# Optimization experiments

Hardware: AMD Instinct MI355X
Metric: run time of the kernel (lower is better)

The kernel has to match this reference:

```python
import jax, jax.numpy as jnp
import numpy as np

NUM_USERS = 100000
NUM_ITEMS = 150000
NUM_BRANDS = 5000
NUM_NODES = NUM_USERS + NUM_ITEMS + NUM_BRANDS
EMBED_DIM = 64
N_LAYERS = 3
NUM_EDGES = 2000000


def setup_inputs() -> dict:
    key = jax.random.key(0)
    k1, k2, k3, k4, k5, k6 = jax.random.split(key, 6)
    # xavier_uniform bound for Embedding weight [n, d]
    def xavier(k, n, d):
        bound = float(np.sqrt(6.0 / (n + d)))
        return jax.random.uniform(k, (n, d), dtype=jnp.float32, minval=-bound, maxval=bound)
    user_emb = xavier(k1, NUM_USERS, EMBED_DIM)
    item_emb = xavier(k2, NUM_ITEMS, EMBED_DIM)
    brand_emb = xavier(k3, NUM_BRANDS, EMBED_DIM)
    adj_rows = jax.random.randint(k4, (NUM_EDGES,), 0, NUM_NODES, dtype=jnp.int32)
    adj_cols = jax.random.randint(k5, (NUM_EDGES,), 0, NUM_NODES, dtype=jnp.int32)
    # normalized adjacency values (positive, small), as in sym-normalized LightGCN adj
    adj_vals = jax.random.uniform(k6, (NUM_EDGES,), dtype=jnp.float32) * 0.1
    return {
        "user_emb": user_emb,
        "item_emb": item_emb,
        "brand_emb": brand_emb,
        "adj_rows": adj_rows,
        "adj_cols": adj_cols,
        "adj_vals": adj_vals,
    }


def _spmm(rows, cols, vals, x):
    # y[r] = sum_{e: rows[e]==r} vals[e] * x[cols[e]]
    msgs = vals[:, None] * x[cols]  # [E, D]
    return jax.ops.segment_sum(msgs, rows, num_segments=NUM_NODES)


def reference(user_emb, item_emb, brand_emb, adj_rows, adj_cols, adj_vals):
    ego = jnp.concatenate([user_emb, item_emb, brand_emb], axis=0)  # [N, D]
    acc = ego  # running sum instead of stack+mean
    for _ in range(N_LAYERS):
        ego = _spmm(adj_rows, adj_cols, adj_vals, ego)
        acc = acc + ego
    final = acc / jnp.float32(N_LAYERS + 1)
    final_user = final[:NUM_USERS]
    final_item = final[NUM_USERS:NUM_USERS + NUM_ITEMS]
    return (final_user, final_item)
```

## Files before the change

kernel.cpp:

```cpp
#include <hip/hip_runtime.h>

#define NUSER 100000
#define NITEM 150000
#define NBRAND 5000
#define NNODES (NUSER + NITEM + NBRAND)
#define DIM 64
#define NOUTROWS (NUSER + NITEM)

#define BINSHIFT 10
#define NBINS ((NNODES + (1 << BINSHIFT) - 1) >> BINSHIFT)
#define EPB 8192
#define CAP 12288

__device__ __forceinline__ float bf2f(unsigned short u) {
    union { unsigned int i; float f; } c;
    c.i = ((unsigned int)u) << 16;
    return c.f;
}
__device__ __forceinline__ unsigned short f2bf(float f) {
    union { float f; unsigned int i; } c;
    c.f = f;
    unsigned int r = c.i + 0x7FFFu + ((c.i >> 16) & 1u);
    return (unsigned short)(r >> 16);
}

__global__ __launch_bounds__(256) void lgcn_binA_init(const int* __restrict__ rows,
                                                      const int* __restrict__ cols,
                                                      const float* __restrict__ vals,
                                                      int* __restrict__ binCnt,
                                                      int2* __restrict__ binned,
                                                      int nedges, int nBinABlocks,
                                                      const float4* __restrict__ u,
                                                      const float4* __restrict__ it,
                                                      const float4* __restrict__ br,
                                                      ushort4* __restrict__ x0b) {
    __shared__ int hist[NBINS];
    __shared__ int base[NBINS];
    if (blockIdx.x >= nBinABlocks) {
        int i = (blockIdx.x - nBinABlocks) * 256 + threadIdx.x;
        const int total = NNODES * (DIM / 4);
        if (i >= total) return;
        float4 v;
        if (i < NUSER * (DIM / 4)) {
            v = u[i];
        } else if (i < (NUSER + NITEM) * (DIM / 4)) {
            v = it[i - NUSER * (DIM / 4)];
        } else {
            v = br[i - (NUSER + NITEM) * (DIM / 4)];
        }
        ushort4 o;
        o.x = f2bf(v.x); o.y = f2bf(v.y); o.z = f2bf(v.z); o.w = f2bf(v.w);
        x0b[i] = o;
        return;
    }
    for (int i = threadIdx.x; i < NBINS; i += 256) hist[i] = 0;
    __syncthreads();
    int beg = blockIdx.x * EPB;
    int end = beg + EPB;
    if (end > nedges) end = nedges;
    for (int e = beg + threadIdx.x; e < end; e += 256) {
        atomicAdd(&hist[rows[e] >> BINSHIFT], 1);
    }
    __syncthreads();
    for (int i = threadIdx.x; i < NBINS; i += 256) {
        int h = hist[i];
        base[i] = h ? (i * CAP + atomicAdd(&binCnt[i], h)) : 0;
        hist[i] = 0;
    }
    __syncthreads();
    for (int e = beg + threadIdx.x; e < end; e += 256) {
        int r = rows[e];
        int b = r >> BINSHIFT;
        int pos = base[b] + atomicAdd(&hist[b], 1);
        int2 p;
        p.x = ((r & ((1 << BINSHIFT) - 1)) << 18) | cols[e];
        p.y = __float_as_int(vals[e]);
        binned[pos] = p;
    }
}

__global__ __launch_bounds__(256) void lgcn_binscan(const int* __restrict__ binCnt,
                                                    int* __restrict__ binScan,
                                                    int* __restrict__ rowptr, int nedges) {
    __shared__ int lds[256];
    int t = threadIdx.x;
    int v = (t < NBINS) ? binCnt[t] : 0;
    lds[t] = v;
    __syncthreads();
    for (int off = 1; off < 256; off <<= 1) {
        int s = (t >= off) ? lds[t - off] : 0;
        __syncthreads();
        lds[t] += s;
        __syncthreads();
    }
    if (t < NBINS) binScan[t] = lds[t] - v;
    if (t == 0) rowptr[NNODES] = nedges;
}

__global__ __launch_bounds__(256) void lgcn_binB(const int* __restrict__ binCnt,
                                                 const int* __restrict__ binScan,
                                                 const int2* __restrict__ binned,
                                                 int2* __restrict__ colval,
                                                 int* __restrict__ rowptr) {
    __shared__ int lhist[1024];
    __shared__ int lcur[1024];
    __shared__ int part[256];
    int b = blockIdx.x;
    int t = threadIdx.x;
    int cnt = binCnt[b];
    int gbase = binScan[b];
    int rbeg = b << BINSHIFT;
    int nrows = NNODES - rbeg;
    if (nrows > 1024) nrows = 1024;
    #pragma unroll
    for (int k = 0; k < 4; ++k) lhist[t + 256 * k] = 0;
    __syncthreads();
    const int2* bsrc = binned + (size_t)b * CAP;
    for (int e = t; e < cnt; e += 256) {
        atomicAdd(&lhist[bsrc[e].x >> 18], 1);
    }
    __syncthreads();
    int h0 = lhist[4 * t + 0];
    int h1 = lhist[4 * t + 1];
    int h2 = lhist[4 * t + 2];
    int h3 = lhist[4 * t + 3];
    int tot = h0 + h1 + h2 + h3;
    part[t] = tot;
    __syncthreads();
    for (int off = 1; off < 256; off <<= 1) {
        int v = (t >= off) ? part[t - off] : 0;
        __syncthreads();
        part[t] += v;
        __syncthreads();
    }
    int c0 = gbase + part[t] - tot;
    int c1 = c0 + h0;
    int c2 = c1 + h1;
    int c3 = c2 + h2;
    lcur[4 * t + 0] = c0;
    lcur[4 * t + 1] = c1;
    lcur[4 * t + 2] = c2;
    lcur[4 * t + 3] = c3;
    if (4 * t + 0 < nrows) rowptr[rbeg + 4 * t + 0] = c0;
    if (4 * t + 1 < nrows) rowptr[rbeg + 4 * t + 1] = c1;
    if (4 * t + 2 < nrows) rowptr[rbeg + 4 * t + 2] = c2;
    if (4 * t + 3 < nrows) rowptr[rbeg + 4 * t + 3] = c3;
    __syncthreads();
    for (int e = t; e < cnt; e += 256) {
        int2 p = bsrc[e];
        int lr = p.x >> 18;
        int pos = atomicAdd(&lcur[lr], 1);
        int2 cv;
        cv.x = p.x & 0x3FFFF;
        cv.y = p.y;
        colval[pos] = cv;
    }
}

template <bool FINAL>
__global__ __launch_bounds__(256) void lgcn_spmm_csr(const int* __restrict__ row_ptr,
                                                     const int2* __restrict__ colval,
                                                     const ushort4* __restrict__ xb,
                                                     ushort4* __restrict__ yb,
                                                     const ushort4* __restrict__ x0b,
                                                     const ushort4* __restrict__ y1b,
                                                     const ushort4* __restrict__ y2b,
                                                     float4* __restrict__ out) {
    int t = blockIdx.x * blockDim.x + threadIdx.x;
    int row = t >> 4;
    int l = t & 15;
    if (FINAL) { if (row >= NOUTROWS) return; }
    else       { if (row >= NNODES) return; }
    int beg = row_ptr[row];
    int end = row_ptr[row + 1];
    float4 s = make_float4(0.f, 0.f, 0.f, 0.f);
    int p = beg;
    while (p + 8 <= end) {
        int2 cv[8];
        ushort4 a[8];
        #pragma unroll
        for (int k = 0; k < 8; ++k) cv[k] = colval[p + k];
        #pragma unroll
        for (int k = 0; k < 8; ++k) a[k] = xb[(size_t)cv[k].x * (DIM / 4) + l];
        #pragma unroll
        for (int k = 0; k < 8; ++k) {
            float v = __int_as_float(cv[k].y);
            s.x += v * bf2f(a[k].x); s.y += v * bf2f(a[k].y);
            s.z += v * bf2f(a[k].z); s.w += v * bf2f(a[k].w);
        }
        p += 8;
    }
    if (p + 4 <= end) {
        int2 cv[4];
        ushort4 a[4];
        #pragma unroll
        for (int k = 0; k < 4; ++k) cv[k] = colval[p + k];
        #pragma unroll
        for (int k = 0; k < 4; ++k) a[k] = xb[(size_t)cv[k].x * (DIM / 4) + l];
        #pragma unroll
        for (int k = 0; k < 4; ++k) {
            float v = __int_as_float(cv[k].y);
            s.x += v * bf2f(a[k].x); s.y += v * bf2f(a[k].y);
            s.z += v * bf2f(a[k].z); s.w += v * bf2f(a[k].w);
        }
        p += 4;
    }
    if (p + 2 <= end) {
        int2 cv0 = colval[p];
        int2 cv1 = colval[p + 1];
        ushort4 a0 = xb[(size_t)cv0.x * (DIM / 4) + l];
        ushort4 a1 = xb[(size_t)cv1.x * (DIM / 4) + l];
        float v0 = __int_as_float(cv0.y);
        float v1 = __int_as_float(cv1.y);
        s.x += v0 * bf2f(a0.x); s.y += v0 * bf2f(a0.y);
        s.z += v0 * bf2f(a0.z); s.w += v0 * bf2f(a0.w);
        s.x += v1 * bf2f(a1.x); s.y += v1 * bf2f(a1.y);
        s.z += v1 * bf2f(a1.z); s.w += v1 * bf2f(a1.w);
        p += 2;
    }
    if (p < end) {
        int2 cv = colval[p];
        ushort4 a = xb[(size_t)cv.x * (DIM / 4) + l];
        float v = __int_as_float(cv.y);
        s.x += v * bf2f(a.x); s.y += v * bf2f(a.y);
        s.z += v * bf2f(a.z); s.w += v * bf2f(a.w);
    }
    size_t off = (size_t)row * (DIM / 4) + l;
    if (!FINAL) {
        ushort4 o;
        o.x = f2bf(s.x); o.y = f2bf(s.y); o.z = f2bf(s.z); o.w = f2bf(s.w);
        yb[off] = o;
    } else {
        ushort4 x0 = x0b[off];
        ushort4 a1 = y1b[off];
        ushort4 a2 = y2b[off];
        float4 r;
        r.x = (bf2f(x0.x) + bf2f(a1.x) + bf2f(a2.x) + s.x) * 0.25f;
        r.y = (bf2f(x0.y) + bf2f(a1.y) + bf2f(a2.y) + s.y) * 0.25f;
        r.z = (bf2f(x0.z) + bf2f(a1.z) + bf2f(a2.z) + s.z) * 0.25f;
        r.w = (bf2f(x0.w) + bf2f(a1.w) + bf2f(a2.w) + s.w) * 0.25f;
        out[off] = r;
    }
}


static inline size_t align256(size_t x) { return (x + 255) & ~(size_t)255; }

extern "C" void kernel_launch(void* const* d_in, const int* in_sizes, int n_in,
                              void* d_out, int out_size, void* d_ws, size_t ws_size,
                              hipStream_t stream) {
    const float4* u  = (const float4*)d_in[0];
    const float4* it = (const float4*)d_in[1];
    const float4* br = (const float4*)d_in[2];
    const int*   rows = (const int*)d_in[3];
    const int*   cols = (const int*)d_in[4];
    const float* vals = (const float*)d_in[5];
    const int nedges = in_sizes[3];
    float4* out = (float4*)d_out;

    char* ws = (char*)d_ws;
    size_t o = 0;
    ushort4* x0b   = (ushort4*)(ws + o); o = align256(o + (size_t)NNODES * DIM * 2);
    ushort4* y1b   = (ushort4*)(ws + o); o = align256(o + (size_t)NNODES * DIM * 2);
    ushort4* y2b   = (ushort4*)(ws + o); o = align256(o + (size_t)NNODES * DIM * 2);
    int*   rowptr  = (int*)(ws + o);     o = align256(o + (size_t)(NNODES + 1) * 4);
    int*   binCnt  = (int*)(ws + o);     o = align256(o + 256 * 4);
    int*   binScan = (int*)(ws + o);     o = align256(o + 256 * 4);
    int2*  colval  = (int2*)(ws + o);    o = align256(o + (size_t)nedges * 8);

    int2* binned = (int2*)y1b;

    const int THREADS = 256;
    const int vecTotal = NNODES * (DIM / 4);
    const int vecBlocks = (vecTotal + THREADS - 1) / THREADS;
    const int spmmBlocks = (NNODES * 16 + THREADS - 1) / THREADS;
    const int finalBlocks = (NOUTROWS * 16 + THREADS - 1) / THREADS;
    const int binABlocks = (nedges + EPB - 1) / EPB;

    hipMemsetAsync(binCnt, 0, 256 * 4, stream);
    lgcn_binA_init<<<binABlocks + vecBlocks, THREADS, 0, stream>>>(
        rows, cols, vals, binCnt, binned, nedges, binABlocks, u, it, br, x0b);
    lgcn_binscan<<<1, THREADS, 0, stream>>>(binCnt, binScan, rowptr, nedges);
    lgcn_binB<<<NBINS, THREADS, 0, stream>>>(binCnt, binScan, binned, colval, rowptr);

    lgcn_spmm_csr<false><<<spmmBlocks, THREADS, 0, stream>>>(rowptr, colval, x0b, y1b,
                                                             nullptr, nullptr, nullptr, nullptr);
    lgcn_spmm_csr<false><<<spmmBlocks, THREADS, 0, stream>>>(rowptr, colval, y1b, y2b,
                                                             nullptr, nullptr, nullptr, nullptr);
    lgcn_spmm_csr<true><<<finalBlocks, THREADS, 0, stream>>>(rowptr, colval, y2b, nullptr,
                                                             x0b, y1b, y2b, out);
}
```

Baseline: 238.6 us.

## Fold bin scan into binB, split init kernel, register-cache rows in binA

Removes the single-block bin-scan kernel; every binB block now does its own redundant 256-entry scan of the bin counts in shared memory. The fp32-to-bf16 conversion of the embeddings moves out of the binning kernel into its own launch after binB. binA now handles 4096 edges per block and keeps each thread's 16 row indices in registers, so rows are read from memory only once. This saves a launch and a global read pass, at the cost of an extra init launch, more binA blocks contending on the global bin counters, and repeated scan work in every binB block.

```diff
diff --git a/kernel.cpp b/kernel.cpp
--- a/kernel.cpp
+++ b/kernel.cpp
@@ -9,7 +9,7 @@
 
 #define BINSHIFT 10
 #define NBINS ((NNODES + (1 << BINSHIFT) - 1) >> BINSHIFT)
-#define EPB 8192
+#define EPB 4096
 #define CAP 12288
 
 __device__ __forceinline__ float bf2f(unsigned short u) {
@@ -24,42 +24,25 @@
     return (unsigned short)(r >> 16);
 }
 
-__global__ __launch_bounds__(256) void lgcn_binA_init(const int* __restrict__ rows,
-                                                      const int* __restrict__ cols,
-                                                      const float* __restrict__ vals,
-                                                      int* __restrict__ binCnt,
-                                                      int2* __restrict__ binned,
-                                                      int nedges, int nBinABlocks,
-                                                      const float4* __restrict__ u,
-                                                      const float4* __restrict__ it,
-                                                      const float4* __restrict__ br,
-                                                      ushort4* __restrict__ x0b) {
+__global__ __launch_bounds__(256) void lgcn_binA(const int* __restrict__ rows,
+                                                 const int* __restrict__ cols,
+                                                 const float* __restrict__ vals,
+                                                 int* __restrict__ binCnt,
+                                                 int2* __restrict__ binned,
+                                                 int nedges) {
     __shared__ int hist[NBINS];
     __shared__ int base[NBINS];
-    if (blockIdx.x >= nBinABlocks) {
-        int i = (blockIdx.x - nBinABlocks) * 256 + threadIdx.x;
-        const int total = NNODES * (DIM / 4);
-        if (i >= total) return;
-        float4 v;
-        if (i < NUSER * (DIM / 4)) {
-            v = u[i];
-        } else if (i < (NUSER + NITEM) * (DIM / 4)) {
-            v = it[i - NUSER * (DIM / 4)];
-        } else {
-            v = br[i - (NUSER + NITEM) * (DIM / 4)];
-        }
-        ushort4 o;
-        o.x = f2bf(v.x); o.y = f2bf(v.y); o.z = f2bf(v.z); o.w = f2bf(v.w);
-        x0b[i] = o;
-        return;
-    }
     for (int i = threadIdx.x; i < NBINS; i += 256) hist[i] = 0;
     __syncthreads();
     int beg = blockIdx.x * EPB;
     int end = beg + EPB;
     if (end > nedges) end = nedges;
-    for (int e = beg + threadIdx.x; e < end; e += 256) {
-        atomicAdd(&hist[rows[e] >> BINSHIFT], 1);
+    int r[16];
+    #pragma unroll
+    for (int k = 0; k < 16; ++k) {
+        int e = beg + threadIdx.x + k * 256;
+        r[k] = (e < end) ? rows[e] : -1;
+        if (r[k] >= 0) atomicAdd(&hist[r[k] >> BINSHIFT], 1);
     }
     __syncthreads();
     for (int i = threadIdx.x; i < NBINS; i += 256) {
@@ -68,53 +51,48 @@
         hist[i] = 0;
     }
     __syncthreads();
-    for (int e = beg + threadIdx.x; e < end; e += 256) {
-        int r = rows[e];
-        int b = r >> BINSHIFT;
-        int pos = base[b] + atomicAdd(&hist[b], 1);
-        int2 p;
-        p.x = ((r & ((1 << BINSHIFT) - 1)) << 18) | cols[e];
-        p.y = __float_as_int(vals[e]);
-        binned[pos] = p;
-    }
-}
-
-__global__ __launch_bounds__(256) void lgcn_binscan(const int* __restrict__ binCnt,
-                                                    int* __restrict__ binScan,
-                                                    int* __restrict__ rowptr, int nedges) {
-    __shared__ int lds[256];
-    int t = threadIdx.x;
-    int v = (t < NBINS) ? binCnt[t] : 0;
-    lds[t] = v;
-    __syncthreads();
-    for (int off = 1; off < 256; off <<= 1) {
-        int s = (t >= off) ? lds[t - off] : 0;
-        __syncthreads();
-        lds[t] += s;
-        __syncthreads();
-    }
-    if (t < NBINS) binScan[t] = lds[t] - v;
-    if (t == 0) rowptr[NNODES] = nedges;
+    #pragma unroll
+    for (int k = 0; k < 16; ++k) {
+        int e = beg + threadIdx.x + k * 256;
+        if (r[k] >= 0) {
+            int b = r[k] >> BINSHIFT;
+            int pos = base[b] + atomicAdd(&hist[b], 1);
+            int2 p;
+            p.x = ((r[k] & ((1 << BINSHIFT) - 1)) << 18) | cols[e];
+            p.y = __float_as_int(vals[e]);
+            binned[pos] = p;
+        }
+    }
 }
 
 __global__ __launch_bounds__(256) void lgcn_binB(const int* __restrict__ binCnt,
-                                                 const int* __restrict__ binScan,
                                                  const int2* __restrict__ binned,
                                                  int2* __restrict__ colval,
-                                                 int* __restrict__ rowptr) {
+                                                 int* __restrict__ rowptr,
+                                                 int nedges) {
     __shared__ int lhist[1024];
     __shared__ int lcur[1024];
     __shared__ int part[256];
+    __shared__ int sScan[256];
     int b = blockIdx.x;
     int t = threadIdx.x;
+    int v = (t < NBINS) ? binCnt[t] : 0;
+    sScan[t] = v;
+    #pragma unroll
+    for (int k = 0; k < 4; ++k) lhist[t + 256 * k] = 0;
+    __syncthreads();
+    for (int off = 1; off < 256; off <<= 1) {
+        int s2 = (t >= off) ? sScan[t - off] : 0;
+        __syncthreads();
+        sScan[t] += s2;
+        __syncthreads();
+    }
     int cnt = binCnt[b];
-    int gbase = binScan[b];
+    int gbase = sScan[b] - cnt;
+    if (b == 0 && t == 0) rowptr[NNODES] = nedges;
     int rbeg = b << BINSHIFT;
     int nrows = NNODES - rbeg;
     if (nrows > 1024) nrows = 1024;
-    #pragma unroll
-    for (int k = 0; k < 4; ++k) lhist[t + 256 * k] = 0;
-    __syncthreads();
     const int2* bsrc = binned + (size_t)b * CAP;
     for (int e = t; e < cnt; e += 256) {
         atomicAdd(&lhist[bsrc[e].x >> 18], 1);
@@ -128,9 +106,9 @@
     part[t] = tot;
     __syncthreads();
     for (int off = 1; off < 256; off <<= 1) {
-        int v = (t >= off) ? part[t - off] : 0;
-        __syncthreads();
-        part[t] += v;
+        int v2 = (t >= off) ? part[t - off] : 0;
+        __syncthreads();
+        part[t] += v2;
         __syncthreads();
     }
     int c0 = gbase + part[t] - tot;
@@ -155,6 +133,27 @@
         cv.y = p.y;
         colval[pos] = cv;
     }
+}
+
+
+__global__ __launch_bounds__(256) void lgcn_init(const float4* __restrict__ u,
+                                                 const float4* __restrict__ it,
+                                                 const float4* __restrict__ br,
+                                                 ushort4* __restrict__ x0b) {
+    int i = blockIdx.x * blockDim.x + threadIdx.x;
+    const int total = NNODES * (DIM / 4);
+    if (i >= total) return;
+    float4 v;
+    if (i < NUSER * (DIM / 4)) {
+        v = u[i];
+    } else if (i < (NUSER + NITEM) * (DIM / 4)) {
+        v = it[i - NUSER * (DIM / 4)];
+    } else {
+        v = br[i - (NUSER + NITEM) * (DIM / 4)];
+    }
+    ushort4 o;
+    o.x = f2bf(v.x); o.y = f2bf(v.y); o.z = f2bf(v.z); o.w = f2bf(v.w);
+    x0b[i] = o;
 }
 
 template <bool FINAL>
@@ -265,7 +264,6 @@
     ushort4* y2b   = (ushort4*)(ws + o); o = align256(o + (size_t)NNODES * DIM * 2);
     int*   rowptr  = (int*)(ws + o);     o = align256(o + (size_t)(NNODES + 1) * 4);
     int*   binCnt  = (int*)(ws + o);     o = align256(o + 256 * 4);
-    int*   binScan = (int*)(ws + o);     o = align256(o + 256 * 4);
     int2*  colval  = (int2*)(ws + o);    o = align256(o + (size_t)nedges * 8);
 
     int2* binned = (int2*)y1b;
@@ -278,10 +276,10 @@
     const int binABlocks = (nedges + EPB - 1) / EPB;
 
     hipMemsetAsync(binCnt, 0, 256 * 4, stream);
-    lgcn_binA_init<<<binABlocks + vecBlocks, THREADS, 0, stream>>>(
-        rows, cols, vals, binCnt, binned, nedges, binABlocks, u, it, br, x0b);
-    lgcn_binscan<<<1, THREADS, 0, stream>>>(binCnt, binScan, rowptr, nedges);
-    lgcn_binB<<<NBINS, THREADS, 0, stream>>>(binCnt, binScan, binned, colval, rowptr);
+    lgcn_binA<<<binABlocks, THREADS, 0, stream>>>(rows, cols, vals, binCnt, binned, nedges);
+    lgcn_binB<<<NBINS, THREADS, 0, stream>>>(binCnt, binned, colval, rowptr, nedges);
+
+    lgcn_init<<<vecBlocks, THREADS, 0, stream>>>(u, it, br, x0b);
 
     lgcn_spmm_csr<false><<<spmmBlocks, THREADS, 0, stream>>>(rowptr, colval, x0b, y1b,
                                                              nullptr, nullptr, nullptr, nullptr);
```

Measured after the change: 255.8 us. +7.2%, slower.
